# Kernel optimization log

Hardware: AMD Instinct MI355X
Metric: run time of the kernel (lower is better)

Reference implementation:

```python
import jax, jax.numpy as jnp
import numpy as np

N_NODES = 50000
N_EDGES = 800000
NUM_FEATURES = 128
DIM = 32
HEADS = 16
NUM_CLASSES = 2
NUM_GRAPHS = 64


def setup_inputs() -> dict:
    key = jax.random.key(0)
    ks = jax.random.split(key, 16)
    inv = lambda fan_in: 1.0 / np.sqrt(fan_in)
    inp = {
        "x": jax.random.normal(ks[0], (N_NODES, NUM_FEATURES), dtype=jnp.float32),
        "edge_index": jax.random.randint(ks[1], (2, N_EDGES), 0, N_NODES, dtype=jnp.int64),
        "batch": jnp.sort(jax.random.randint(ks[2], (N_NODES,), 0, NUM_GRAPHS, dtype=jnp.int64)),
        # conv1: GraphConv(num_features -> dim)
        "W1_rel": jax.random.uniform(ks[3], (NUM_FEATURES, DIM), jnp.float32, -inv(NUM_FEATURES), inv(NUM_FEATURES)),
        "b1_rel": jnp.zeros((DIM,), jnp.float32),
        "W1_root": jax.random.uniform(ks[4], (NUM_FEATURES, DIM), jnp.float32, -inv(NUM_FEATURES), inv(NUM_FEATURES)),
        # conv3: GATConv(dim -> dim, heads=16, concat)
        "Wg": jax.random.uniform(ks[5], (DIM, HEADS * DIM), jnp.float32, -inv(DIM), inv(DIM)),
        "att_src": jax.random.uniform(ks[6], (HEADS, DIM), jnp.float32, -inv(DIM), inv(DIM)),
        "att_dst": jax.random.uniform(ks[7], (HEADS, DIM), jnp.float32, -inv(DIM), inv(DIM)),
        "bg": jnp.zeros((HEADS * DIM,), jnp.float32),
        # conv5: GraphConv(dim*16 -> dim)
        "W5_rel": jax.random.uniform(ks[8], (HEADS * DIM, DIM), jnp.float32, -inv(HEADS * DIM), inv(HEADS * DIM)),
        "b5_rel": jnp.zeros((DIM,), jnp.float32),
        "W5_root": jax.random.uniform(ks[9], (HEADS * DIM, DIM), jnp.float32, -inv(HEADS * DIM), inv(HEADS * DIM)),
        # fc1, fc2
        "Wfc1": jax.random.uniform(ks[10], (DIM, DIM), jnp.float32, -inv(DIM), inv(DIM)),
        "bfc1": jnp.zeros((DIM,), jnp.float32),
        "Wfc2": jax.random.uniform(ks[11], (DIM, NUM_CLASSES), jnp.float32, -inv(DIM), inv(DIM)),
        "bfc2": jnp.zeros((NUM_CLASSES,), jnp.float32),
    }
    return inp


def _graph_conv(x, src, dst, W_rel, b_rel, W_root):
    # PyG GraphConv (aggr='add'): out = lin_rel(sum_{j->i} x_j) + lin_root(x_i)
    agg = jax.ops.segment_sum(x[src], dst, num_segments=N_NODES)
    return agg @ W_rel + b_rel + x @ W_root


def _gat_conv(x, src, dst, W, att_src, att_dst, b):
    # PyG GATConv with add_self_loops=True, concat=True, negative_slope=0.2.
    # Dropout on attention is inactive in eval mode.
    loops = jnp.arange(N_NODES, dtype=src.dtype)
    src = jnp.concatenate([src, loops])
    dst = jnp.concatenate([dst, loops])
    h = (x @ W).reshape(N_NODES, HEADS, DIM)            # [N,H,C]
    a_src = jnp.einsum("nhc,hc->nh", h, att_src)        # [N,H]
    a_dst = jnp.einsum("nhc,hc->nh", h, att_dst)
    e = jax.nn.leaky_relu(a_src[src] + a_dst[dst], 0.2)  # [E,H]
    # segment softmax over incoming edges of each destination node
    e_max = jax.ops.segment_max(e, dst, num_segments=N_NODES)
    e_max = jnp.where(jnp.isfinite(e_max), e_max, 0.0)
    ex = jnp.exp(e - e_max[dst])
    denom = jax.ops.segment_sum(ex, dst, num_segments=N_NODES)
    alpha = ex / (denom[dst] + 1e-16)                   # [E,H]
    out = jax.ops.segment_sum(alpha[:, :, None] * h[src], dst, num_segments=N_NODES)
    return out.reshape(N_NODES, HEADS * DIM) + b


def reference(x, edge_index, batch, W1_rel, b1_rel, W1_root, Wg, att_src, att_dst, bg,
              W5_rel, b5_rel, W5_root, Wfc1, bfc1, Wfc2, bfc2):
    src, dst = edge_index[0], edge_index[1]
    h = jax.nn.relu(_graph_conv(x, src, dst, W1_rel, b1_rel, W1_root))
    h = jax.nn.relu(_gat_conv(h, src, dst, Wg, att_src, att_dst, bg))
    h = jax.nn.relu(_graph_conv(h, src, dst, W5_rel, b5_rel, W5_root))
    g = jax.ops.segment_sum(h, batch, num_segments=NUM_GRAPHS)  # global_add_pool
    g = jax.nn.relu(g @ Wfc1 + bfc1)
    logits = g @ Wfc2 + bfc2
    return jax.nn.sigmoid(logits)
```

## Files before the change

kernel.cpp:

```cpp
#include <hip/hip_runtime.h>
#include <stdint.h>

#define N_NODES 50000
#define N_EDGES 800000
#define NFEAT 128
#define DIM 32
#define HEADS 16
#define NGRAPH 64

__device__ inline int clampN(int v) {
    return v < 0 ? 0 : (v >= N_NODES ? N_NODES - 1 : v);
}

__device__ inline float lrelu(float e) { return e < 0.f ? 0.2f * e : e; }

__device__ inline bool edges_are_i64(const int* raw) {
    int acc = 0;
#pragma unroll
    for (int i = 1; i < 16; i += 2) acc |= raw[2 * N_EDGES - 16 + i];
    return acc == 0;
}

__global__ __launch_bounds__(256) void decode_edges_hist(const int* __restrict__ raw,
                                                         int* __restrict__ esrc,
                                                         int* __restrict__ edst,
                                                         int* __restrict__ deg) {
    const bool is64 = edges_are_i64(raw);
    int e = blockIdx.x * 256 + threadIdx.x;
    if (e < N_EDGES) {
        int s, d;
        if (is64) { s = raw[2 * e]; d = raw[2 * (N_EDGES + e)]; }
        else      { s = raw[e];     d = raw[N_EDGES + e]; }
        s = clampN(s); d = clampN(d);
        esrc[e] = s; edst[e] = d;
        atomicAdd(&deg[d], 1);
    }
}

__global__ __launch_bounds__(256) void decode_batch(const int* __restrict__ raw,
                                                    int* __restrict__ out) {
    int acc = 0;
#pragma unroll
    for (int i = 1; i < 16; i += 2) acc |= raw[N_NODES - 16 + i];
    const bool is64 = (acc == 0);
    int b = blockIdx.x * 256 + threadIdx.x;
    if (b < N_NODES) {
        int v = is64 ? raw[2 * b] : raw[b];
        out[b] = v < 0 ? 0 : (v >= NGRAPH ? NGRAPH - 1 : v);
    }
}

__global__ __launch_bounds__(256) void init_kernel(int* __restrict__ deg, float* __restrict__ gpool) {
    int i = blockIdx.x * 256 + threadIdx.x;
    if (i < N_NODES) deg[i] = 1;
    if (i < NGRAPH * DIM) gpool[i] = 0.f;
}

__global__ __launch_bounds__(1024) void scan_kernel(const int* __restrict__ deg,
                                                    int* __restrict__ off, int* __restrict__ cur) {
    __shared__ int part[1024];
    const int t = threadIdx.x;
    const int CH = (N_NODES + 1023) / 1024;
    int b0 = t * CH, b1 = b0 + CH;
    if (b0 > N_NODES) b0 = N_NODES;
    if (b1 > N_NODES) b1 = N_NODES;
    int s = 0;
    for (int i = b0; i < b1; ++i) s += deg[i];
    part[t] = s;
    __syncthreads();
    for (int ofs = 1; ofs < 1024; ofs <<= 1) {
        int v = part[t];
        int u = (t >= ofs) ? part[t - ofs] : 0;
        __syncthreads();
        part[t] = v + u;
        __syncthreads();
    }
    int run = (t > 0) ? part[t - 1] : 0;
    for (int i = b0; i < b1; ++i) { off[i] = run; cur[i] = run; run += deg[i]; }
    if (t == 1023) off[N_NODES] = part[1023];
}

__global__ __launch_bounds__(256) void place_kernel(const int* __restrict__ esrc,
                                                    const int* __restrict__ edst,
                                                    int* __restrict__ cur, int* __restrict__ nbr) {
    int idx = blockIdx.x * 256 + threadIdx.x;
    if (idx >= N_EDGES + N_NODES) return;
    int d, v;
    if (idx < N_EDGES) { d = edst[idx]; v = esrc[idx]; }
    else { d = idx - N_EDGES; v = d; }
    int p = atomicAdd(&cur[d], 1);
    nbr[p] = v;
}

__global__ __launch_bounds__(256) void node_linear2(const float* __restrict__ x,
                                                    const float* __restrict__ Wa,
                                                    const float* __restrict__ Wb,
                                                    const float* __restrict__ bias_b,
                                                    float* __restrict__ xrb, int n) {
    constexpr int KC = 128;
    constexpr int NB = 8;
    __shared__ float sWt[2][32][KC + 4];
    __shared__ float sX[NB][KC];
    const int t = threadIdx.x;
    const int o = t & 63;
    const int mat = o >> 5;
    const int c = o & 31;
    const int sub = t >> 6;
    const int base = blockIdx.x * NB;

    for (int i = t; i < 2 * KC * 32; i += 256) {
        int m = i >= KC * 32;
        int j = i - m * KC * 32;
        int kk = j >> 5, cc = j & 31;
        sWt[m][cc][kk] = (m ? Wb : Wa)[kk * 32 + cc];
    }
    for (int i = t; i < NB * KC; i += 256) {
        int r = i >> 7, kk = i & (KC - 1);
        int node = base + r;
        sX[r][kk] = (node < n) ? x[(size_t)node * KC + kk] : 0.f;
    }
    __syncthreads();
    float acc[2] = {0.f, 0.f};
#pragma unroll 4
    for (int kv = 0; kv < KC / 4; ++kv) {
        const float4 w = *(const float4*)&sWt[mat][c][kv * 4];
#pragma unroll
        for (int s = 0; s < 2; ++s) {
            const float4 xv = *(const float4*)&sX[sub + s * 4][kv * 4];
            acc[s] += w.x * xv.x + w.y * xv.y + w.z * xv.z + w.w * xv.w;
        }
    }
    const float bb = (mat == 1) ? bias_b[c] : 0.f;
#pragma unroll
    for (int s = 0; s < 2; ++s) {
        int node = base + sub + s * 4;
        if (node < n) xrb[(size_t)node * 64 + mat * 32 + c] = acc[s] + bb;
    }
}

__global__ __launch_bounds__(256) void graphconv_gather(const float* __restrict__ xrb,
                                                        const int* __restrict__ off,
                                                        const int* __restrict__ nbr,
                                                        float* __restrict__ out) {
    int d = blockIdx.x * 4 + (threadIdx.x >> 6);
    if (d >= N_NODES) return;
    const int l = threadIdx.x & 63;
    const int c = l & 31, half = l >> 5;
    const int j0 = off[d], j1 = off[d + 1];
    float acc = 0.f;
    int j = j0 + half;
    for (; j + 6 < j1; j += 8) {
        int s0 = nbr[j], s1 = nbr[j + 2], s2 = nbr[j + 4], s3 = nbr[j + 6];
        float v0 = xrb[(size_t)s0 * 64 + c];
        float v1 = xrb[(size_t)s1 * 64 + c];
        float v2 = xrb[(size_t)s2 * 64 + c];
        float v3 = xrb[(size_t)s3 * 64 + c];
        acc += (v0 + v1) + (v2 + v3);
    }
    for (; j < j1; j += 2) acc += xrb[(size_t)nbr[j] * 64 + c];
    acc += __shfl_xor(acc, 32);
    acc += xrb[(size_t)d * 64 + 32 + c] - xrb[(size_t)d * 64 + c];
    if (half == 0) out[(size_t)d * 32 + c] = acc > 0.f ? acc : 0.f;
}

__global__ __launch_bounds__(1024) void attc_kernel(const float* __restrict__ Wg,
                                                    const float* __restrict__ attS,
                                                    const float* __restrict__ attD,
                                                    float* __restrict__ attc) {
    const int t = threadIdx.x;
    const int sd = t >> 9, k = (t >> 4) & 31, hd = t & 15;
    const float* att = sd ? attD : attS;
    float acc = 0.f;
#pragma unroll
    for (int c = 0; c < 32; ++c) acc += Wg[k * 512 + hd * 32 + c] * att[hd * 32 + c];
    attc[t] = acc;
}

__global__ __launch_bounds__(256) void gat_att(const float* __restrict__ h1,
                                               const float* __restrict__ attc,
                                               float* __restrict__ asrc,
                                               float* __restrict__ adst) {
    __shared__ float sh1[8][32];
    __shared__ float sattc[1024];
    const int t = threadIdx.x;
    for (int i = t; i < 1024; i += 256) sattc[i] = attc[i];
    {
        int n0 = t >> 5, k = t & 31;
        sh1[n0][k] = h1[(size_t)(blockIdx.x * 8 + n0) * 32 + k];
    }
    __syncthreads();
    const int nl = t >> 5, hd = (t >> 1) & 15, sd = t & 1;
    float acc = 0.f;
#pragma unroll
    for (int k = 0; k < 32; ++k) acc += sh1[nl][k] * sattc[sd * 512 + k * 16 + hd];
    (sd ? adst : asrc)[(size_t)(blockIdx.x * 8 + nl) * 16 + hd] = acc;
}

__global__ __launch_bounds__(256) void gat_gather(const float* __restrict__ h1,
                                                  const float* __restrict__ asrc,
                                                  const float* __restrict__ adst,
                                                  const int* __restrict__ off,
                                                  const int* __restrict__ nbr,
                                                  float* __restrict__ agg) {
    const int d = blockIdx.x * 4 + (threadIdx.x >> 6);
    const int l = threadIdx.x & 63;
    const int hd = l >> 2;
    const int kb = (l & 3) << 3;
    const float adst_v = adst[(size_t)d * 16 + hd];
    const int j0 = off[d], j1 = off[d + 1];

    float m = -1e30f;
    int j = j0;
    for (; j + 4 <= j1; j += 4) {
        int s0 = nbr[j], s1 = nbr[j + 1], s2 = nbr[j + 2], s3 = nbr[j + 3];
        float e0 = lrelu(asrc[(size_t)s0 * 16 + hd] + adst_v);
        float e1 = lrelu(asrc[(size_t)s1 * 16 + hd] + adst_v);
        float e2 = lrelu(asrc[(size_t)s2 * 16 + hd] + adst_v);
        float e3 = lrelu(asrc[(size_t)s3 * 16 + hd] + adst_v);
        m = fmaxf(m, fmaxf(fmaxf(e0, e1), fmaxf(e2, e3)));
    }
    for (; j < j1; ++j)
        m = fmaxf(m, lrelu(asrc[(size_t)nbr[j] * 16 + hd] + adst_v));

    float den = 0.f;
    float a0x = 0.f, a0y = 0.f, a0z = 0.f, a0w = 0.f;
    float a1x = 0.f, a1y = 0.f, a1z = 0.f, a1w = 0.f;
    j = j0;
    for (; j + 2 <= j1; j += 2) {
        int s0 = nbr[j], s1 = nbr[j + 1];
        float e0 = lrelu(asrc[(size_t)s0 * 16 + hd] + adst_v);
        float e1 = lrelu(asrc[(size_t)s1 * 16 + hd] + adst_v);
        float ex0 = expf(e0 - m), ex1 = expf(e1 - m);
        den += ex0 + ex1;
        const float4 h00 = *(const float4*)&h1[(size_t)s0 * 32 + kb];
        const float4 h01 = *(const float4*)&h1[(size_t)s0 * 32 + kb + 4];
        const float4 h10 = *(const float4*)&h1[(size_t)s1 * 32 + kb];
        const float4 h11 = *(const float4*)&h1[(size_t)s1 * 32 + kb + 4];
        a0x += ex0 * h00.x + ex1 * h10.x; a0y += ex0 * h00.y + ex1 * h10.y;
        a0z += ex0 * h00.z + ex1 * h10.z; a0w += ex0 * h00.w + ex1 * h10.w;
        a1x += ex0 * h01.x + ex1 * h11.x; a1y += ex0 * h01.y + ex1 * h11.y;
        a1z += ex0 * h01.z + ex1 * h11.z; a1w += ex0 * h01.w + ex1 * h11.w;
    }
    if (j < j1) {
        int s0 = nbr[j];
        float e0 = lrelu(asrc[(size_t)s0 * 16 + hd] + adst_v);
        float ex0 = expf(e0 - m);
        den += ex0;
        const float4 h00 = *(const float4*)&h1[(size_t)s0 * 32 + kb];
        const float4 h01 = *(const float4*)&h1[(size_t)s0 * 32 + kb + 4];
        a0x += ex0 * h00.x; a0y += ex0 * h00.y; a0z += ex0 * h00.z; a0w += ex0 * h00.w;
        a1x += ex0 * h01.x; a1y += ex0 * h01.y; a1z += ex0 * h01.z; a1w += ex0 * h01.w;
    }
    const float r = 1.f / (den + 1e-16f);
    float* ap = agg + (size_t)d * 512 + 8 * l;
    float4 o0 = {a0x * r, a0y * r, a0z * r, a0w * r};
    float4 o1 = {a1x * r, a1y * r, a1z * r, a1w * r};
    *(float4*)ap = o0;
    *(float4*)(ap + 4) = o1;
}

__global__ __launch_bounds__(512) void gat_ffn(const float* __restrict__ agg,
                                               const float* __restrict__ Wg,
                                               const float* __restrict__ bg,
                                               const float* __restrict__ W5_rel,
                                               const float* __restrict__ W5_root,
                                               const float* __restrict__ b5,
                                               float* __restrict__ xrb) {
    __shared__ float sA[8][512];
    __shared__ float sH[8][512];
    const int t = threadIdx.x;
    const int base = blockIdx.x * 8;

    {
        const float4* av = (const float4*)(agg + (size_t)base * 512);
        float4* sv = (float4*)&sA[0][0];
        sv[t] = av[t];
        sv[t + 512] = av[t + 512];
    }
    __syncthreads();

    {
        const int hh = (t >> 5) << 5;
        float acc[8] = {0.f, 0.f, 0.f, 0.f, 0.f, 0.f, 0.f, 0.f};
        for (int k = 0; k < 32; ++k) {
            const float wv = Wg[k * 512 + t];
#pragma unroll
            for (int nl = 0; nl < 8; ++nl) acc[nl] += sA[nl][hh + k] * wv;
        }
        const float bgv = bg[t];
#pragma unroll
        for (int nl = 0; nl < 8; ++nl) {
            float v = acc[nl] + bgv;
            sH[nl][t] = v > 0.f ? v : 0.f;
        }
    }
    __syncthreads();

    float* spart = &sA[0][0];
    const int w = t >> 6, l = t & 63;
    {
        const float* wp = (l < 32) ? (W5_rel + l) : (W5_root + (l - 32));
        float p[8] = {0.f, 0.f, 0.f, 0.f, 0.f, 0.f, 0.f, 0.f};
        const int c0 = w * 64;
        for (int cc = 0; cc < 64; ++cc) {
            const int col = c0 + cc;
            const float wv = wp[(size_t)col * 32];
#pragma unroll
            for (int nl = 0; nl < 8; ++nl) p[nl] += sH[nl][col] * wv;
        }
#pragma unroll
        for (int nl = 0; nl < 8; ++nl) spart[(size_t)(w * 8 + nl) * 64 + l] = p[nl];
    }
    __syncthreads();

    {
        float acc = (l >= 32) ? b5[l - 32] : 0.f;
#pragma unroll
        for (int ww = 0; ww < 8; ++ww) acc += spart[(size_t)(ww * 8 + w) * 64 + l];
        xrb[(size_t)(base + w) * 64 + l] = acc;
    }
}

__global__ __launch_bounds__(512) void gat_mega(const float* __restrict__ h1,
                                                const float* __restrict__ asrc,
                                                const float* __restrict__ adst,
                                                const int* __restrict__ off,
                                                const int* __restrict__ nbr,
                                                const float* __restrict__ Wg,
                                                const float* __restrict__ bg,
                                                const float* __restrict__ W5_rel,
                                                const float* __restrict__ W5_root,
                                                const float* __restrict__ b5,
                                                float* __restrict__ xrb) {
    __shared__ float sh_agg[8][512];
    __shared__ float sh_h2[8][512];
    const int t = threadIdx.x;
    const int w = t >> 6, l = t & 63;
    const int d = blockIdx.x * 8 + w;

    {
        const int hd = l >> 2;
        const int kb = (l & 3) << 3;
        const float adst_v = adst[(size_t)d * 16 + hd];
        const int j0 = off[d], j1 = off[d + 1];
        float m = -1e30f;
        int j = j0;
        for (; j + 4 <= j1; j += 4) {
            int s0 = nbr[j], s1 = nbr[j + 1], s2 = nbr[j + 2], s3 = nbr[j + 3];
            float e0 = lrelu(asrc[(size_t)s0 * 16 + hd] + adst_v);
            float e1 = lrelu(asrc[(size_t)s1 * 16 + hd] + adst_v);
            float e2 = lrelu(asrc[(size_t)s2 * 16 + hd] + adst_v);
            float e3 = lrelu(asrc[(size_t)s3 * 16 + hd] + adst_v);
            m = fmaxf(m, fmaxf(fmaxf(e0, e1), fmaxf(e2, e3)));
        }
        for (; j < j1; ++j)
            m = fmaxf(m, lrelu(asrc[(size_t)nbr[j] * 16 + hd] + adst_v));

        float den = 0.f;
        float a0x = 0.f, a0y = 0.f, a0z = 0.f, a0w = 0.f;
        float a1x = 0.f, a1y = 0.f, a1z = 0.f, a1w = 0.f;
        j = j0;
        for (; j + 2 <= j1; j += 2) {
            int s0 = nbr[j], s1 = nbr[j + 1];
            float e0 = lrelu(asrc[(size_t)s0 * 16 + hd] + adst_v);
            float e1 = lrelu(asrc[(size_t)s1 * 16 + hd] + adst_v);
            float ex0 = expf(e0 - m), ex1 = expf(e1 - m);
            den += ex0 + ex1;
            const float4 h00 = *(const float4*)&h1[(size_t)s0 * 32 + kb];
            const float4 h01 = *(const float4*)&h1[(size_t)s0 * 32 + kb + 4];
            const float4 h10 = *(const float4*)&h1[(size_t)s1 * 32 + kb];
            const float4 h11 = *(const float4*)&h1[(size_t)s1 * 32 + kb + 4];
            a0x += ex0 * h00.x + ex1 * h10.x; a0y += ex0 * h00.y + ex1 * h10.y;
            a0z += ex0 * h00.z + ex1 * h10.z; a0w += ex0 * h00.w + ex1 * h10.w;
            a1x += ex0 * h01.x + ex1 * h11.x; a1y += ex0 * h01.y + ex1 * h11.y;
            a1z += ex0 * h01.z + ex1 * h11.z; a1w += ex0 * h01.w + ex1 * h11.w;
        }
        if (j < j1) {
            int s0 = nbr[j];
            float e0 = lrelu(asrc[(size_t)s0 * 16 + hd] + adst_v);
            float ex0 = expf(e0 - m);
            den += ex0;
            const float4 h00 = *(const float4*)&h1[(size_t)s0 * 32 + kb];
            const float4 h01 = *(const float4*)&h1[(size_t)s0 * 32 + kb + 4];
            a0x += ex0 * h00.x; a0y += ex0 * h00.y; a0z += ex0 * h00.z; a0w += ex0 * h00.w;
            a1x += ex0 * h01.x; a1y += ex0 * h01.y; a1z += ex0 * h01.z; a1w += ex0 * h01.w;
        }
        const float r = 1.f / (den + 1e-16f);
        float* ap = &sh_agg[w][8 * l];
        ap[0] = a0x * r; ap[1] = a0y * r; ap[2] = a0z * r; ap[3] = a0w * r;
        ap[4] = a1x * r; ap[5] = a1y * r; ap[6] = a1z * r; ap[7] = a1w * r;
    }
    __syncthreads();

    {
        const int hh = (t >> 5) << 5;
        float acc[8] = {0.f, 0.f, 0.f, 0.f, 0.f, 0.f, 0.f, 0.f};
        for (int k = 0; k < 32; ++k) {
            const float wv = Wg[k * 512 + t];
#pragma unroll
            for (int nl = 0; nl < 8; ++nl) acc[nl] += sh_agg[nl][hh + k] * wv;
        }
        const float bgv = bg[t];
#pragma unroll
        for (int nl = 0; nl < 8; ++nl) {
            float v = acc[nl] + bgv;
            sh_h2[nl][t] = v > 0.f ? v : 0.f;
        }
    }
    __syncthreads();

    float* spart = &sh_agg[0][0];
    {
        const float* wp = (l < 32) ? (W5_rel + l) : (W5_root + (l - 32));
        float p[8] = {0.f, 0.f, 0.f, 0.f, 0.f, 0.f, 0.f, 0.f};
        const int c0 = w * 64;
        for (int cc = 0; cc < 64; ++cc) {
            const int col = c0 + cc;
            const float wv = wp[(size_t)col * 32];
#pragma unroll
            for (int nl = 0; nl < 8; ++nl) p[nl] += sh_h2[nl][col] * wv;
        }
#pragma unroll
        for (int nl = 0; nl < 8; ++nl) spart[(size_t)(w * 8 + nl) * 64 + l] = p[nl];
    }
    __syncthreads();

    {
        float acc = (l >= 32) ? b5[l - 32] : 0.f;
#pragma unroll
        for (int ww = 0; ww < 8; ++ww) acc += spart[(size_t)(ww * 8 + w) * 64 + l];
        xrb[(size_t)(blockIdx.x * 8 + w) * 64 + l] = acc;
    }
}

__global__ __launch_bounds__(256) void pool_kernel(const float* __restrict__ h3,
                                                   const int* __restrict__ batch,
                                                   float* __restrict__ g) {
    const int KRUN = 32;
    int c = threadIdx.x & 31;
    int grp = blockIdx.x * 8 + (threadIdx.x >> 5);
    int n0 = grp * KRUN;
    if (n0 >= N_NODES) return;
    int nend = n0 + KRUN;
    if (nend > N_NODES) nend = N_NODES;
    float acc = 0.f;
    int curb = -1;
    for (int nn = n0; nn < nend; ++nn) {
        int b = batch[nn];
        if (b != curb) {
            if (curb >= 0) atomicAdd(&g[curb * 32 + c], acc);
            acc = 0.f;
            curb = b;
        }
        acc += h3[(size_t)nn * 32 + c];
    }
    if (curb >= 0) atomicAdd(&g[curb * 32 + c], acc);
}

__global__ __launch_bounds__(256) void final_head(const float* __restrict__ g,
                                                  const float* __restrict__ Wfc1,
                                                  const float* __restrict__ bfc1,
                                                  const float* __restrict__ Wfc2,
                                                  const float* __restrict__ bfc2,
                                                  float* __restrict__ out) {
    __shared__ float sg[NGRAPH * 32];
    __shared__ float s1[NGRAPH * 32];
    const int t = threadIdx.x;
    for (int i = t; i < NGRAPH * 32; i += 256) sg[i] = g[i];
    __syncthreads();
    for (int i = t; i < NGRAPH * 32; i += 256) {
        int gi = i >> 5, c = i & 31;
        float acc = bfc1[c];
#pragma unroll
        for (int k = 0; k < 32; ++k) acc += sg[gi * 32 + k] * Wfc1[k * 32 + c];
        s1[i] = acc > 0.f ? acc : 0.f;
    }
    __syncthreads();
    if (t < NGRAPH * 2) {
        int gi = t >> 1, cls = t & 1;
        float acc = bfc2[cls];
#pragma unroll
        for (int k = 0; k < 32; ++k) acc += s1[gi * 32 + k] * Wfc2[k * 2 + cls];
        out[t] = 1.f / (1.f + expf(-acc));
    }
}

extern "C" void kernel_launch(void* const* d_in, const int* in_sizes, int n_in,
                              void* d_out, int out_size, void* d_ws, size_t ws_size,
                              hipStream_t stream) {
    const float* x       = (const float*)d_in[0];
    const int*   eraw    = (const int*)d_in[1];
    const int*   braw    = (const int*)d_in[2];
    const float* W1_rel  = (const float*)d_in[3];
    const float* b1_rel  = (const float*)d_in[4];
    const float* W1_root = (const float*)d_in[5];
    const float* Wg      = (const float*)d_in[6];
    const float* attS    = (const float*)d_in[7];
    const float* attD    = (const float*)d_in[8];
    const float* bg      = (const float*)d_in[9];
    const float* W5_rel  = (const float*)d_in[10];
    const float* b5_rel  = (const float*)d_in[11];
    const float* W5_root = (const float*)d_in[12];
    const float* Wfc1    = (const float*)d_in[13];
    const float* bfc1    = (const float*)d_in[14];
    const float* Wfc2    = (const float*)d_in[15];
    const float* bfc2    = (const float*)d_in[16];
    float* out = (float*)d_out;

    float* f     = (float*)d_ws;
    float* xrb   = f;
    float* h1    = xrb + (size_t)N_NODES * 64;
    float* asrc  = h1 + (size_t)N_NODES * 32;
    float* adst  = asrc + (size_t)N_NODES * 16;
    float* attc  = adst + (size_t)N_NODES * 16;
    float* gpool = attc + 1024;
    int* esrcd   = (int*)(gpool + 2048);
    int* edstd   = esrcd + N_EDGES;
    int* batchd  = edstd + N_EDGES;
    int* deg     = batchd + N_NODES;
    int* off     = deg + (N_NODES + 1);
    int* cur     = off + (N_NODES + 1);
    int* nbr     = cur + N_NODES;
    uintptr_t aggp = (uintptr_t)(nbr + (N_EDGES + N_NODES));
    aggp = (aggp + 15) & ~(uintptr_t)15;
    float* agg = (float*)aggp;
    const size_t need_split = (aggp - (uintptr_t)d_ws) + (size_t)N_NODES * 512 * 4;
    const bool use_split = ws_size >= need_split;

    init_kernel<<<(N_NODES + 255) / 256, 256, 0, stream>>>(deg, gpool);
    decode_edges_hist<<<(N_EDGES + 255) / 256, 256, 0, stream>>>(eraw, esrcd, edstd, deg);
    decode_batch<<<(N_NODES + 255) / 256, 256, 0, stream>>>(braw, batchd);
    scan_kernel<<<1, 1024, 0, stream>>>(deg, off, cur);
    place_kernel<<<(N_EDGES + N_NODES + 255) / 256, 256, 0, stream>>>(esrcd, edstd, cur, nbr);

    node_linear2<<<(N_NODES + 7) / 8, 256, 0, stream>>>(x, W1_rel, W1_root, b1_rel, xrb, N_NODES);
    graphconv_gather<<<(N_NODES + 3) / 4, 256, 0, stream>>>(xrb, off, nbr, h1);

    attc_kernel<<<1, 1024, 0, stream>>>(Wg, attS, attD, attc);
    gat_att<<<(N_NODES + 7) / 8, 256, 0, stream>>>(h1, attc, asrc, adst);
    if (use_split) {
        gat_gather<<<(N_NODES + 3) / 4, 256, 0, stream>>>(h1, asrc, adst, off, nbr, agg);
        gat_ffn<<<N_NODES / 8, 512, 0, stream>>>(agg, Wg, bg, W5_rel, W5_root, b5_rel, xrb);
    } else {
        gat_mega<<<N_NODES / 8, 512, 0, stream>>>(h1, asrc, adst, off, nbr, Wg, bg,
                                                  W5_rel, W5_root, b5_rel, xrb);
    }

    graphconv_gather<<<(N_NODES + 3) / 4, 256, 0, stream>>>(xrb, off, nbr, h1);

    pool_kernel<<<((N_NODES + 31) / 32 + 7) / 8, 256, 0, stream>>>(h1, batchd, gpool);
    final_head<<<1, 256, 0, stream>>>(gpool, Wfc1, bfc1, Wfc2, bfc2, out);
}
```

Measured before the change: 696.4 us.

## Register-tile gat_ffn over 16 nodes with float4 weights and swizzled LDS

Reworks the post-GAT feed-forward kernel so each block handles 16 nodes instead of 8. Each thread now computes a 4x4 register tile with float4 weight loads, and XOR-swizzled LDS layouts avoid bank conflicts. This raises reuse of the weight loads and cuts global weight traffic per node. The cost is 64KB of LDS per block, which limits occupancy, and the grid becomes N_NODES/16, which divides exactly only because N_NODES=50000.

```diff
diff --git a/kernel.cpp b/kernel.cpp
--- a/kernel.cpp
+++ b/kernel.cpp
@@ -266,58 +266,103 @@
                                                const float* __restrict__ W5_root,
                                                const float* __restrict__ b5,
                                                float* __restrict__ xrb) {
-    __shared__ float sA[8][512];
-    __shared__ float sH[8][512];
-    const int t = threadIdx.x;
-    const int base = blockIdx.x * 8;
-
-    {
-        const float4* av = (const float4*)(agg + (size_t)base * 512);
-        float4* sv = (float4*)&sA[0][0];
-        sv[t] = av[t];
-        sv[t + 512] = av[t + 512];
-    }
-    __syncthreads();
-
-    {
-        const int hh = (t >> 5) << 5;
-        float acc[8] = {0.f, 0.f, 0.f, 0.f, 0.f, 0.f, 0.f, 0.f};
+    __shared__ float lds[16384];
+    float* sA = lds;
+    float* sH = lds + 8192;
+    const int t = threadIdx.x;
+    const int base = blockIdx.x * 16;
+
+    {
+        const float4* src = (const float4*)(agg + (size_t)base * 512);
+#pragma unroll
+        for (int r = 0; r < 4; ++r) {
+            const int i = r * 512 + t;
+            const int n = i >> 7;
+            const int c4 = (i & 127) << 2;
+            const int hd = c4 >> 5;
+            const int k0 = c4 & 31;
+            *(float4*)&sA[n * 512 + hd * 32 + (k0 ^ ((hd & 7) << 2))] = src[i];
+        }
+    }
+    __syncthreads();
+
+    {
+        const int cg = t & 127;
+        const int col0 = cg << 2;
+        const int hd = col0 >> 5;
+        const int nb = (t >> 7) << 2;
+        const int abase = hd * 32;
+        const int swz = (hd & 7) << 2;
+        float4 acc[4];
+#pragma unroll
+        for (int i = 0; i < 4; ++i) acc[i] = make_float4(0.f, 0.f, 0.f, 0.f);
         for (int k = 0; k < 32; ++k) {
-            const float wv = Wg[k * 512 + t];
-#pragma unroll
-            for (int nl = 0; nl < 8; ++nl) acc[nl] += sA[nl][hh + k] * wv;
-        }
-        const float bgv = bg[t];
-#pragma unroll
-        for (int nl = 0; nl < 8; ++nl) {
-            float v = acc[nl] + bgv;
-            sH[nl][t] = v > 0.f ? v : 0.f;
-        }
-    }
-    __syncthreads();
-
-    float* spart = &sA[0][0];
-    const int w = t >> 6, l = t & 63;
-    {
-        const float* wp = (l < 32) ? (W5_rel + l) : (W5_root + (l - 32));
-        float p[8] = {0.f, 0.f, 0.f, 0.f, 0.f, 0.f, 0.f, 0.f};
-        const int c0 = w * 64;
-        for (int cc = 0; cc < 64; ++cc) {
-            const int col = c0 + cc;
-            const float wv = wp[(size_t)col * 32];
-#pragma unroll
-            for (int nl = 0; nl < 8; ++nl) p[nl] += sH[nl][col] * wv;
-        }
-#pragma unroll
-        for (int nl = 0; nl < 8; ++nl) spart[(size_t)(w * 8 + nl) * 64 + l] = p[nl];
-    }
-    __syncthreads();
-
-    {
-        float acc = (l >= 32) ? b5[l - 32] : 0.f;
-#pragma unroll
-        for (int ww = 0; ww < 8; ++ww) acc += spart[(size_t)(ww * 8 + w) * 64 + l];
-        xrb[(size_t)(base + w) * 64 + l] = acc;
+            const float4 w = *(const float4*)&Wg[k * 512 + col0];
+            const int ao = abase + (k ^ swz);
+#pragma unroll
+            for (int i = 0; i < 4; ++i) {
+                const float a = sA[(nb + i) * 512 + ao];
+                acc[i].x += a * w.x; acc[i].y += a * w.y;
+                acc[i].z += a * w.z; acc[i].w += a * w.w;
+            }
+        }
+        const float4 bb = *(const float4*)&bg[col0];
+#pragma unroll
+        for (int i = 0; i < 4; ++i) {
+            float4 v;
+            v.x = fmaxf(acc[i].x + bb.x, 0.f);
+            v.y = fmaxf(acc[i].y + bb.y, 0.f);
+            v.z = fmaxf(acc[i].z + bb.z, 0.f);
+            v.w = fmaxf(acc[i].w + bb.w, 0.f);
+            const int n = nb + i;
+            *(float4*)&sH[n * 512 + (col0 ^ ((n & 7) << 2))] = v;
+        }
+    }
+    __syncthreads();
+
+    {
+        const int s = t >> 6;
+        const int ng = (t >> 4) & 3;
+        const int lg = t & 15;
+        const int l0 = lg << 2;
+        const float* wb = (l0 < 32) ? (W5_rel + l0) : (W5_root + (l0 - 32));
+        const int nb = ng << 2;
+        float4 o[4];
+#pragma unroll
+        for (int i = 0; i < 4; ++i) o[i] = make_float4(0.f, 0.f, 0.f, 0.f);
+        const int cbase = s << 6;
+        for (int cq = 0; cq < 16; ++cq) {
+            const int c = cbase + (cq << 2);
+            const float4 w0 = *(const float4*)&wb[(size_t)(c + 0) * 32];
+            const float4 w1 = *(const float4*)&wb[(size_t)(c + 1) * 32];
+            const float4 w2 = *(const float4*)&wb[(size_t)(c + 2) * 32];
+            const float4 w3 = *(const float4*)&wb[(size_t)(c + 3) * 32];
+#pragma unroll
+            for (int i = 0; i < 4; ++i) {
+                const int n = nb + i;
+                const float4 h = *(const float4*)&sH[n * 512 + (c ^ ((n & 7) << 2))];
+                o[i].x += h.x * w0.x + h.y * w1.x + h.z * w2.x + h.w * w3.x;
+                o[i].y += h.x * w0.y + h.y * w1.y + h.z * w2.y + h.w * w3.y;
+                o[i].z += h.x * w0.z + h.y * w1.z + h.z * w2.z + h.w * w3.z;
+                o[i].w += h.x * w0.w + h.y * w1.w + h.z * w2.w + h.w * w3.w;
+            }
+        }
+#pragma unroll
+        for (int i = 0; i < 4; ++i)
+            *(float4*)&lds[(s << 10) + (nb + i) * 64 + l0] = o[i];
+    }
+    __syncthreads();
+
+    {
+#pragma unroll
+        for (int r = 0; r < 2; ++r) {
+            const int idx = (r << 9) + t;
+            const int n = idx >> 6, l = idx & 63;
+            float v = (l >= 32) ? b5[l - 32] : 0.f;
+#pragma unroll
+            for (int ss = 0; ss < 8; ++ss) v += lds[(ss << 10) + n * 64 + l];
+            xrb[(size_t)(base + n) * 64 + l] = v;
+        }
     }
 }
 
@@ -540,7 +585,7 @@
     gat_att<<<(N_NODES + 7) / 8, 256, 0, stream>>>(h1, attc, asrc, adst);
     if (use_split) {
         gat_gather<<<(N_NODES + 3) / 4, 256, 0, stream>>>(h1, asrc, adst, off, nbr, agg);
-        gat_ffn<<<N_NODES / 8, 512, 0, stream>>>(agg, Wg, bg, W5_rel, W5_root, b5_rel, xrb);
+        gat_ffn<<<N_NODES / 16, 512, 0, stream>>>(agg, Wg, bg, W5_rel, W5_root, b5_rel, xrb);
     } else {
         gat_mega<<<N_NODES / 8, 512, 0, stream>>>(h1, asrc, adst, off, nbr, Wg, bg,
                                                   W5_rel, W5_root, b5_rel, xrb);
```

Result: slower. 896.9 us (+28.8%).
